# Optimization experiments

Hardware: AMD Instinct MI355X
Metric: run time of the kernel (lower is better)

## Reference

```python
import jax, jax.numpy as jnp
import numpy as np


def setup_inputs() -> dict:
    key = jax.random.key(0)
    k1, k2, k3, k4, k5 = jax.random.split(key, 5)
    N, M, K = 200000, 50, 4
    T = 1000.0
    ti = jnp.sort(jax.random.uniform(k1, (N,), dtype=jnp.float32) * T)
    mi = jax.random.randint(k2, (N,), 0, M, dtype=jnp.int64)
    mu_at_events = jax.random.uniform(k3, (N,), dtype=jnp.float32) * 0.5 + 0.05
    alpha = jax.random.uniform(k4, (K, M, M), dtype=jnp.float32) * 0.1
    gamma = jax.random.uniform(k5, (K,), dtype=jnp.float32) * 2.0 + 0.5
    return {"ti": ti, "mi": mi, "mu_at_events": mu_at_events, "alpha": alpha, "gamma": gamma}


def _hawkes_logsum(ti, mi, mu_at_events, alpha, gamma):
    # ti: [N] sorted event times; mi: [N] event types in [0, M)
    # alpha: [K, M, M]; gamma: [K]; mu_at_events: [N]
    N = ti.shape[0]
    M = alpha.shape[1]
    # inter-event gaps; dt[0] = 0 so the first event has zero excitation state
    dt = jnp.concatenate([jnp.zeros((1,), ti.dtype), ti[1:] - ti[:-1]])  # [N]
    a = jnp.exp(-gamma[None, :] * dt[:, None])  # [N, K] decay factors
    # one-hot of the PREVIOUS event's type (row 0 is all-zero, matching e_mi)
    prev_onehot = jnp.zeros((N, M), ti.dtype).at[jnp.arange(1, N), mi[:-1]].set(1.0)
    b = a[:, None, :] * prev_onehot[:, :, None]  # [N, M, K]

    # linear recurrence S_i = a_i * S_{i-1} + b_i via associative scan
    # combine((a1,b1),(a2,b2)) = (a1*a2, a2*b1 + b2)
    def combine(x, y):
        a1, b1 = x
        a2, b2 = y
        return (a1 * a2, a2[:, None, :] * b1 + b2)

    _, S = jax.lax.associative_scan(combine, (a, b))  # S: [N, M, K]
    # S[i, m, k] = sum_{j < i, m_j = m} exp(-gamma_k (t_i - t_j))
    alpha_at = alpha[:, mi, :]  # [K, N, M] rows of alpha for each event's type
    lam = mu_at_events + jnp.einsum('knm,nmk,k->n', alpha_at, S, gamma)  # [N]
    return jnp.sum(jnp.log(lam))


def reference(ti, mi, mu_at_events, alpha, gamma):
    return _hawkes_logsum(ti, mi, mu_at_events, alpha, gamma)
```

## Files before the change

kernel.cpp:

```cpp
#include <hip/hip_runtime.h>
#include <hip/hip_bf16.h>

#define CHUNK 256
#define MM 50
#define KK 4
#define STATE (MM*KK)
#define ASTRIDE 51
#define SUP 32
#define NSMAX 26
#define NSUB 8
#define SUBSZ 32

__device__ __forceinline__ unsigned short f2bf(float x) {
  unsigned u = __float_as_uint(x);
  u += 0x7fffu + ((u >> 16) & 1u);
  return (unsigned short)(u >> 16);
}

__global__ __launch_bounds__(256) void phase1(
    const float* __restrict__ ti, const int* __restrict__ mi,
    const float* __restrict__ gamma, float* __restrict__ chunkB,
    float* __restrict__ superB, float* __restrict__ out0, int N, int G) {
  int g = blockIdx.x, tid = threadIdx.x;
  if (g == 0 && tid == 0) out0[0] = 0.f;
  int l = g * CHUNK;
  int r = min(N, l + CHUNK);
  __shared__ float Bs[STATE];
  __shared__ float g4[KK];
  if (tid < STATE) Bs[tid] = 0.f;
  if (tid < KK) g4[tid] = gamma[tid];
  __syncthreads();
  float t_end = ti[r - 1];
  int j0 = (g == 0) ? 0 : (l - 1);
  int j = j0 + tid;
  if (j <= r - 2) {
    int m = mi[j];
    float dt = t_end - ti[j];
    #pragma unroll
    for (int k = 0; k < KK; ++k)
      atomicAdd(&Bs[m * KK + k], __expf(-g4[k] * dt));
  }
  __syncthreads();
  if (tid < STATE) {
    float v = Bs[tid];
    chunkB[(size_t)g * STATE + tid] = v;
    int sup = g / SUP;
    float gk = g4[tid & 3];
    float Tsup = ti[min(N, (sup + 1) * SUP * CHUNK) - 1];
    atomicAdd(&superB[(size_t)sup * STATE + tid], __expf(-gk * (Tsup - t_end)) * v);
  }
}

__global__ __launch_bounds__(512) void phase3(
    const float* __restrict__ ti, const int* __restrict__ mi,
    const float* __restrict__ mu, const float* __restrict__ alpha,
    const float* __restrict__ gamma, const float* __restrict__ chunkB,
    const float* __restrict__ superB, float* __restrict__ out, int N, int G) {
  int g = blockIdx.x, tid = threadIdx.x;
  int l = g * CHUNK;
  int r = min(N, l + CHUNK);
  int cnt = r - l;
  int sup = g / SUP;
  int g0 = sup * SUP;
  int e = tid >> 1;
  int h = tid & 1;

  __shared__ unsigned P0[MM * ASTRIDE];
  __shared__ unsigned P1[MM * ASTRIDE];
  __shared__ __align__(16) float4 Fj[CHUNK];
  __shared__ int   cj[CHUNK];
  __shared__ __align__(16) float Q[NSUB][STATE];
  __shared__ float red8[8];
  __shared__ float teL[SUP];
  __shared__ float tlast[NSMAX];

  float gk0 = gamma[0], gk1 = gamma[1], gk2 = gamma[2], gk3 = gamma[3];

  for (int i = tid; i < NSUB * STATE; i += 512) ((float*)Q)[i] = 0.f;

  for (int idx = tid; idx < MM * MM; idx += 512) {
    int c = idx / MM, cp = idx - c * MM;
    float a0 = gk0 * alpha[idx];
    float a1 = gk1 * alpha[2500 + idx];
    float a2 = gk2 * alpha[5000 + idx];
    float a3 = gk3 * alpha[7500 + idx];
    P0[c * ASTRIDE + cp] = (unsigned)f2bf(a0) | ((unsigned)f2bf(a1) << 16);
    P1[c * ASTRIDE + cp] = (unsigned)f2bf(a2) | ((unsigned)f2bf(a3) << 16);
  }

  if (tid < SUP) {
    int c = g0 + tid;
    if (c < G) teL[tid] = ti[min(N, (c + 1) * CHUNK) - 1];
  } else if (tid >= 64 && tid < 64 + NSMAX) {
    int s = tid - 64;
    if (s < sup) tlast[s] = ti[min(N, (s + 1) * SUP * CHUNK) - 1];
  }

  float t_ref = ti[(g == 0) ? 0 : (l - 1)];
  if (tid < CHUNK) {
    int j = l - 1 + tid;
    bool valid = (j >= 0) && (j <= r - 2);
    float4 myF = make_float4(0.f, 0.f, 0.f, 0.f);
    int myc = 0;
    if (valid) {
      myc = mi[j];
      float tj = ti[j] - t_ref;
      myF = make_float4(__expf(gk0 * tj), __expf(gk1 * tj),
                        __expf(gk2 * tj), __expf(gk3 * tj));
    }
    cj[tid] = myc;
    Fj[tid] = myF;
    __syncthreads();
    if (valid) {
      float* q = &Q[tid >> 5][myc * KK];
      atomicAdd(q + 0, myF.x); atomicAdd(q + 1, myF.y);
      atomicAdd(q + 2, myF.z); atomicAdd(q + 3, myF.w);
    }
  } else {
    __syncthreads();
  }

  float S = 0.f;
  if (tid < STATE) {
    float gk = gamma[tid & 3];
    int nloc = g - g0;
    #pragma unroll 4
    for (int u = 0; u < nloc; ++u)
      S += __expf(-gk * (t_ref - teL[u])) * chunkB[(size_t)(g0 + u) * STATE + tid];
    #pragma unroll 4
    for (int s = 0; s < sup; ++s)
      S += __expf(-gk * (t_ref - tlast[s])) * superB[(size_t)s * STATE + tid];
  }
  __syncthreads();

  if (tid < STATE) {
    float run = S;
    #pragma unroll
    for (int q = 0; q < NSUB; ++q) {
      float t = Q[q][tid];
      Q[q][tid] = run;
      run += t;
    }
  }
  __syncthreads();

  float local = 0.f;
  {
    int c_n = (e < cnt) ? mi[l + e] : 0;
    int rowb = c_n * ASTRIDE;
    const float4* wb = (const float4*)&Q[e >> 5][0];
    float4 acc = make_float4(0.f, 0.f, 0.f, 0.f);
    if (e < cnt) {
      int mlo = h * 25, mhi = mlo + 25;
      #pragma unroll 5
      for (int m = mlo; m < mhi; ++m) {
        unsigned p0 = P0[rowb + m];
        unsigned p1 = P1[rowb + m];
        float4 w = wb[m];
        acc.x += __uint_as_float(p0 << 16)         * w.x;
        acc.y += __uint_as_float(p0 & 0xffff0000u) * w.y;
        acc.z += __uint_as_float(p1 << 16)         * w.z;
        acc.w += __uint_as_float(p1 & 0xffff0000u) * w.w;
      }
      #pragma unroll 4
      for (int s = (e & ~(SUBSZ - 1)) + h; s <= e; s += 2) {
        unsigned p0 = P0[rowb + cj[s]];
        unsigned p1 = P1[rowb + cj[s]];
        float4 f = Fj[s];
        acc.x += __uint_as_float(p0 << 16)         * f.x;
        acc.y += __uint_as_float(p0 & 0xffff0000u) * f.y;
        acc.z += __uint_as_float(p1 << 16)         * f.z;
        acc.w += __uint_as_float(p1 & 0xffff0000u) * f.w;
      }
    }
    acc.x += __shfl_xor(acc.x, 1, 64);
    acc.y += __shfl_xor(acc.y, 1, 64);
    acc.z += __shfl_xor(acc.z, 1, 64);
    acc.w += __shfl_xor(acc.w, 1, 64);
    if (h == 0 && e < cnt) {
      float tn = ti[l + e] - t_ref;
      float lam = mu[l + e]
                + __expf(-gk0 * tn) * acc.x + __expf(-gk1 * tn) * acc.y
                + __expf(-gk2 * tn) * acc.z + __expf(-gk3 * tn) * acc.w;
      local = __logf(lam);
    }
  }
  #pragma unroll
  for (int off = 32; off > 0; off >>= 1)
    local += __shfl_down(local, off, 64);
  if ((tid & 63) == 0) red8[tid >> 6] = local;
  __syncthreads();
  if (tid == 0) {
    float t = 0.f;
    #pragma unroll
    for (int w = 0; w < 8; ++w) t += red8[w];
    atomicAdd(out, t);
  }
}

extern "C" void kernel_launch(void* const* d_in, const int* in_sizes, int n_in,
                              void* d_out, int out_size, void* d_ws, size_t ws_size,
                              hipStream_t stream) {
  const float* ti    = (const float*)d_in[0];
  const int*   mi    = (const int*)d_in[1];
  const float* mu    = (const float*)d_in[2];
  const float* alpha = (const float*)d_in[3];
  const float* gamma = (const float*)d_in[4];
  float* out = (float*)d_out;
  int N = in_sizes[0];
  int G = (N + CHUNK - 1) / CHUNK;

  float* superB = (float*)d_ws;
  float* chunkB = superB + (size_t)NSMAX * STATE;

  phase1<<<G, 256, 0, stream>>>(ti, mi, gamma, chunkB, superB, out, N, G);
  phase3<<<G, 512, 0, stream>>>(ti, mi, mu, alpha, gamma, chunkB, superB, out, N, G);
}
```

Before: 91.07 us.

## Parallelize carry-in state accumulation across 500 threads with early prefetched float4 loads

```diff
diff --git a/kernel.cpp b/kernel.cpp
--- a/kernel.cpp
+++ b/kernel.cpp
@@ -10,6 +10,9 @@
 #define NSMAX 26
 #define NSUB 8
 #define SUBSZ 32
+#define NSL 10
+#define TPS 50
+#define MAXT 6
 
 __device__ __forceinline__ unsigned short f2bf(float x) {
   unsigned u = __float_as_uint(x);
@@ -62,6 +65,7 @@
   int cnt = r - l;
   int sup = g / SUP;
   int g0 = sup * SUP;
+  int nloc = g - g0;
   int e = tid >> 1;
   int h = tid & 1;
 
@@ -70,11 +74,30 @@
   __shared__ __align__(16) float4 Fj[CHUNK];
   __shared__ int   cj[CHUNK];
   __shared__ __align__(16) float Q[NSUB][STATE];
+  __shared__ __align__(16) float4 PRE[NSL][TPS];
   __shared__ float red8[8];
   __shared__ float teL[SUP];
   __shared__ float tlast[NSMAX];
 
   float gk0 = gamma[0], gk1 = gamma[1], gk2 = gamma[2], gk3 = gamma[3];
+
+  int p = tid / TPS, cm = tid - p * TPS;
+  int T = nloc + sup;
+  float4 L[MAXT];
+  int nt = 0;
+  if (tid < NSL * TPS) {
+    #pragma unroll
+    for (int i = 0; i < MAXT; ++i) {
+      int t = p + i * NSL;
+      if (t < T) {
+        const float* src = (t < nloc)
+            ? &chunkB[(size_t)(g0 + t) * STATE + 4 * cm]
+            : &superB[(size_t)(t - nloc) * STATE + 4 * cm];
+        L[i] = *(const float4*)src;
+        nt = i + 1;
+      }
+    }
+  }
 
   for (int i = tid; i < NSUB * STATE; i += 512) ((float*)Q)[i] = 0.f;
 
@@ -97,11 +120,12 @@
   }
 
   float t_ref = ti[(g == 0) ? 0 : (l - 1)];
+  float4 myF = make_float4(0.f, 0.f, 0.f, 0.f);
+  int myc = 0;
+  bool valid = false;
   if (tid < CHUNK) {
     int j = l - 1 + tid;
-    bool valid = (j >= 0) && (j <= r - 2);
-    float4 myF = make_float4(0.f, 0.f, 0.f, 0.f);
-    int myc = 0;
+    valid = (j >= 0) && (j <= r - 2);
     if (valid) {
       myc = mi[j];
       float tj = ti[j] - t_ref;
@@ -110,30 +134,37 @@
     }
     cj[tid] = myc;
     Fj[tid] = myF;
-    __syncthreads();
-    if (valid) {
-      float* q = &Q[tid >> 5][myc * KK];
-      atomicAdd(q + 0, myF.x); atomicAdd(q + 1, myF.y);
-      atomicAdd(q + 2, myF.z); atomicAdd(q + 3, myF.w);
-    }
-  } else {
-    __syncthreads();
-  }
-
-  float S = 0.f;
+  }
+  __syncthreads();
+
+  if (valid) {
+    float* q = &Q[tid >> 5][myc * KK];
+    atomicAdd(q + 0, myF.x); atomicAdd(q + 1, myF.y);
+    atomicAdd(q + 2, myF.z); atomicAdd(q + 3, myF.w);
+  }
+
+  if (tid < NSL * TPS) {
+    float4 acc = make_float4(0.f, 0.f, 0.f, 0.f);
+    #pragma unroll
+    for (int i = 0; i < MAXT; ++i) {
+      if (i < nt) {
+        int t = p + i * NSL;
+        float dt = t_ref - ((t < nloc) ? teL[t] : tlast[t - nloc]);
+        acc.x += __expf(-gk0 * dt) * L[i].x;
+        acc.y += __expf(-gk1 * dt) * L[i].y;
+        acc.z += __expf(-gk2 * dt) * L[i].z;
+        acc.w += __expf(-gk3 * dt) * L[i].w;
+      }
+    }
+    PRE[p][cm] = acc;
+  }
+  __syncthreads();
+
   if (tid < STATE) {
-    float gk = gamma[tid & 3];
-    int nloc = g - g0;
-    #pragma unroll 4
-    for (int u = 0; u < nloc; ++u)
-      S += __expf(-gk * (t_ref - teL[u])) * chunkB[(size_t)(g0 + u) * STATE + tid];
-    #pragma unroll 4
-    for (int s = 0; s < sup; ++s)
-      S += __expf(-gk * (t_ref - tlast[s])) * superB[(size_t)s * STATE + tid];
-  }
-  __syncthreads();
-
-  if (tid < STATE) {
+    const float* pre = (const float*)PRE;
+    float S = 0.f;
+    #pragma unroll
+    for (int pp = 0; pp < NSL; ++pp) S += pre[pp * STATE + tid];
     float run = S;
     #pragma unroll
     for (int q = 0; q < NSUB; ++q) {
```

New measurement: 91.47 us. About the same (+0.4%).

## Replace per-chunk carry summaries with direct intra-superblock event rescan in phase3

Applied to the files above, without the earlier changes.

```diff
diff --git a/kernel.cpp b/kernel.cpp
--- a/kernel.cpp
+++ b/kernel.cpp
@@ -10,6 +10,7 @@
 #define NSMAX 26
 #define NSUB 8
 #define SUBSZ 32
+#define NW 8
 
 __device__ __forceinline__ unsigned short f2bf(float x) {
   unsigned u = __float_as_uint(x);
@@ -17,45 +18,45 @@
   return (unsigned short)(u >> 16);
 }
 
-__global__ __launch_bounds__(256) void phase1(
+__global__ __launch_bounds__(512) void superk(
     const float* __restrict__ ti, const int* __restrict__ mi,
-    const float* __restrict__ gamma, float* __restrict__ chunkB,
-    float* __restrict__ superB, float* __restrict__ out0, int N, int G) {
-  int g = blockIdx.x, tid = threadIdx.x;
-  if (g == 0 && tid == 0) out0[0] = 0.f;
-  int l = g * CHUNK;
-  int r = min(N, l + CHUNK);
-  __shared__ float Bs[STATE];
-  __shared__ float g4[KK];
-  if (tid < STATE) Bs[tid] = 0.f;
-  if (tid < KK) g4[tid] = gamma[tid];
-  __syncthreads();
-  float t_end = ti[r - 1];
-  int j0 = (g == 0) ? 0 : (l - 1);
-  int j = j0 + tid;
-  if (j <= r - 2) {
+    const float* __restrict__ gamma, float* __restrict__ superB,
+    float* __restrict__ out0, int N) {
+  int s = blockIdx.x, tid = threadIdx.x;
+  if (s == 0 && tid == 0) out0[0] = 0.f;
+  __shared__ float SB[NW][STATE];
+  for (int i = tid; i < NW * STATE; i += 512) ((float*)SB)[i] = 0.f;
+  __syncthreads();
+  float gk0 = gamma[0], gk1 = gamma[1], gk2 = gamma[2], gk3 = gamma[3];
+  int base = s * SUP * CHUNK;
+  int lo = (s == 0) ? 0 : base - 1;
+  int end = min(N, base + SUP * CHUNK);
+  int hi = end - 2;
+  float Tsup = ti[end - 1];
+  float* myb = &SB[tid >> 6][0];
+  for (int j = lo + tid; j <= hi; j += 512) {
     int m = mi[j];
-    float dt = t_end - ti[j];
-    #pragma unroll
-    for (int k = 0; k < KK; ++k)
-      atomicAdd(&Bs[m * KK + k], __expf(-g4[k] * dt));
+    float dt = Tsup - ti[j];
+    float* b = myb + m * KK;
+    atomicAdd(b + 0, __expf(-gk0 * dt));
+    atomicAdd(b + 1, __expf(-gk1 * dt));
+    atomicAdd(b + 2, __expf(-gk2 * dt));
+    atomicAdd(b + 3, __expf(-gk3 * dt));
   }
   __syncthreads();
   if (tid < STATE) {
-    float v = Bs[tid];
-    chunkB[(size_t)g * STATE + tid] = v;
-    int sup = g / SUP;
-    float gk = g4[tid & 3];
-    float Tsup = ti[min(N, (sup + 1) * SUP * CHUNK) - 1];
-    atomicAdd(&superB[(size_t)sup * STATE + tid], __expf(-gk * (Tsup - t_end)) * v);
+    float t = 0.f;
+    #pragma unroll
+    for (int w = 0; w < NW; ++w) t += SB[w][tid];
+    superB[(size_t)s * STATE + tid] = t;
   }
 }
 
 __global__ __launch_bounds__(512) void phase3(
     const float* __restrict__ ti, const int* __restrict__ mi,
     const float* __restrict__ mu, const float* __restrict__ alpha,
-    const float* __restrict__ gamma, const float* __restrict__ chunkB,
-    const float* __restrict__ superB, float* __restrict__ out, int N, int G) {
+    const float* __restrict__ gamma, const float* __restrict__ superB,
+    float* __restrict__ out, int N, int G) {
   int g = blockIdx.x, tid = threadIdx.x;
   int l = g * CHUNK;
   int r = min(N, l + CHUNK);
@@ -70,13 +71,14 @@
   __shared__ __align__(16) float4 Fj[CHUNK];
   __shared__ int   cj[CHUNK];
   __shared__ __align__(16) float Q[NSUB][STATE];
+  __shared__ float SLOC[NW][STATE];
   __shared__ float red8[8];
-  __shared__ float teL[SUP];
   __shared__ float tlast[NSMAX];
 
   float gk0 = gamma[0], gk1 = gamma[1], gk2 = gamma[2], gk3 = gamma[3];
 
   for (int i = tid; i < NSUB * STATE; i += 512) ((float*)Q)[i] = 0.f;
+  for (int i = tid; i < NW * STATE; i += 512) ((float*)SLOC)[i] = 0.f;
 
   for (int idx = tid; idx < MM * MM; idx += 512) {
     int c = idx / MM, cp = idx - c * MM;
@@ -88,20 +90,18 @@
     P1[c * ASTRIDE + cp] = (unsigned)f2bf(a2) | ((unsigned)f2bf(a3) << 16);
   }
 
-  if (tid < SUP) {
-    int c = g0 + tid;
-    if (c < G) teL[tid] = ti[min(N, (c + 1) * CHUNK) - 1];
-  } else if (tid >= 64 && tid < 64 + NSMAX) {
+  if (tid >= 64 && tid < 64 + NSMAX) {
     int s = tid - 64;
     if (s < sup) tlast[s] = ti[min(N, (s + 1) * SUP * CHUNK) - 1];
   }
 
   float t_ref = ti[(g == 0) ? 0 : (l - 1)];
+  float4 myF = make_float4(0.f, 0.f, 0.f, 0.f);
+  int myc = 0;
+  bool valid = false;
   if (tid < CHUNK) {
     int j = l - 1 + tid;
-    bool valid = (j >= 0) && (j <= r - 2);
-    float4 myF = make_float4(0.f, 0.f, 0.f, 0.f);
-    int myc = 0;
+    valid = (j >= 0) && (j <= r - 2);
     if (valid) {
       myc = mi[j];
       float tj = ti[j] - t_ref;
@@ -110,30 +110,39 @@
     }
     cj[tid] = myc;
     Fj[tid] = myF;
-    __syncthreads();
-    if (valid) {
-      float* q = &Q[tid >> 5][myc * KK];
-      atomicAdd(q + 0, myF.x); atomicAdd(q + 1, myF.y);
-      atomicAdd(q + 2, myF.z); atomicAdd(q + 3, myF.w);
-    }
-  } else {
-    __syncthreads();
-  }
-
-  float S = 0.f;
+  }
+  __syncthreads();
+
+  if (valid) {
+    float* q = &Q[tid >> 5][myc * KK];
+    atomicAdd(q + 0, myF.x); atomicAdd(q + 1, myF.y);
+    atomicAdd(q + 2, myF.z); atomicAdd(q + 3, myF.w);
+  }
+
+  {
+    int jlo = (g0 == 0) ? 0 : g0 * CHUNK - 1;
+    int jhi = l - 2;
+    float* myb = &SLOC[tid >> 6][0];
+    for (int j = jlo + tid; j <= jhi; j += 512) {
+      int m = mi[j];
+      float dt = t_ref - ti[j];
+      float* b = myb + m * KK;
+      atomicAdd(b + 0, __expf(-gk0 * dt));
+      atomicAdd(b + 1, __expf(-gk1 * dt));
+      atomicAdd(b + 2, __expf(-gk2 * dt));
+      atomicAdd(b + 3, __expf(-gk3 * dt));
+    }
+  }
+  __syncthreads();
+
   if (tid < STATE) {
     float gk = gamma[tid & 3];
-    int nloc = g - g0;
-    #pragma unroll 4
-    for (int u = 0; u < nloc; ++u)
-      S += __expf(-gk * (t_ref - teL[u])) * chunkB[(size_t)(g0 + u) * STATE + tid];
+    float S = 0.f;
+    #pragma unroll
+    for (int w = 0; w < NW; ++w) S += SLOC[w][tid];
     #pragma unroll 4
     for (int s = 0; s < sup; ++s)
       S += __expf(-gk * (t_ref - tlast[s])) * superB[(size_t)s * STATE + tid];
-  }
-  __syncthreads();
-
-  if (tid < STATE) {
     float run = S;
     #pragma unroll
     for (int q = 0; q < NSUB; ++q) {
@@ -209,10 +218,10 @@
   float* out = (float*)d_out;
   int N = in_sizes[0];
   int G = (N + CHUNK - 1) / CHUNK;
+  int nS = (G + SUP - 1) / SUP;
 
   float* superB = (float*)d_ws;
-  float* chunkB = superB + (size_t)NSMAX * STATE;
-
-  phase1<<<G, 256, 0, stream>>>(ti, mi, gamma, chunkB, superB, out, N, G);
-  phase3<<<G, 512, 0, stream>>>(ti, mi, mu, alpha, gamma, chunkB, superB, out, N, G);
-}
+
+  superk<<<nS, 512, 0, stream>>>(ti, mi, gamma, superB, out, N);
+  phase3<<<G, 512, 0, stream>>>(ti, mi, mu, alpha, gamma, superB, out, N, G);
+}
```

New measurement: 240.4 us. 2.64x slower.
